# Performance work log

Measured on AMD Instinct MI355X. Metric: run time of the kernel, lower is better.

Reference implementation:

```python
import jax, jax.numpy as jnp
import numpy as np
from jax import lax

H = 12  # num_heads

def conv1d_same(x, w, b):
    # x: [B, Cin, L], w: [Cout, Cin, K] (torch Conv1d layout), 'same' padding
    y = lax.conv_general_dilated(x, w, window_strides=(1,), padding='SAME',
                                 dimension_numbers=('NCH', 'OIH', 'NCH'))
    return y + b[None, :, None]

def setup_inputs() -> dict:
    key = jax.random.key(0)
    ks = jax.random.split(key, 16)
    B, N, C = 8, 4096, 768
    d = C // H
    s = 0.02
    return {
        'x': jax.random.normal(ks[0], (B, N, C), dtype=jnp.float32),
        'qkv_w': jax.random.normal(ks[1], (3 * C, C), dtype=jnp.float32) * s,
        'proj_w': jax.random.normal(ks[2], (C, C), dtype=jnp.float32) * s,
        'proj_b': jnp.zeros((C,), dtype=jnp.float32),
        'conv_w': jax.random.normal(ks[3], (d, d, 5), dtype=jnp.float32) * s,  # k=5 from log2(768)
        'conv_b': jnp.zeros((d,), dtype=jnp.float32),
        'fc_w': jax.random.normal(ks[4], (d, d), dtype=jnp.float32) * s,
        'fc_b': jnp.zeros((d,), dtype=jnp.float32),
        'dw1_w': jax.random.normal(ks[5], (d, d, 3), dtype=jnp.float32) * s,
        'dw1_b': jnp.zeros((d,), dtype=jnp.float32),
        'dw2_w': jax.random.normal(ks[6], (d, d, 5), dtype=jnp.float32) * s,
        'dw2_b': jnp.zeros((d,), dtype=jnp.float32),
    }

def reference(x, qkv_w, proj_w, proj_b, conv_w, conv_b, fc_w, fc_b, dw1_w, dw1_b, dw2_w, dw2_b):
    B, N, C = x.shape
    d = C // H
    scale = d ** (-0.5)
    # qkv projection -> [3, B, H, N, d]
    qkv = (x @ qkv_w.T).reshape(B, N, 3, H, d).transpose(2, 0, 3, 1, 4)
    q, k, v = qkv[0], qkv[1], qkv[2]
    # SE-style gate: global avg over tokens, conv over channel axis, sigmoid
    res = jnp.mean(v, axis=2).reshape(B * H, d, 1)          # [BH, d, 1]
    res = conv1d_same(res, conv_w, conv_b)                   # [BH, d, 1]
    res = jax.nn.sigmoid(res).transpose(0, 2, 1).reshape(B, H, 1, d)
    # value branch: two 1D convs over token axis (channels = head_dim)
    vch = v.reshape(B * H, N, d).transpose(0, 2, 1)          # [BH, d, N]
    v2 = conv1d_same(vch, dw1_w, dw1_b) + conv1d_same(vch, dw2_w, dw2_b)
    v2 = v2.transpose(0, 2, 1).reshape(B, H, N, d)
    # channel attention: (scaled k)^T @ q -> [B, H, d, d]
    kq = jnp.einsum('bhnd,bhne->bhde', k * scale, q)
    a = jax.nn.relu(kq) @ fc_w.T + fc_b
    a = jax.nn.softmax(a + kq, axis=-1)
    # (a @ v2^T)^T -> [B, H, N, d]
    out = jnp.einsum('bhde,bhne->bhnd', a, v2)
    out = res * out
    out = out.transpose(0, 2, 1, 3).reshape(B, N, C)
    return out @ proj_w.T + proj_b
```

## Files before the change

### kernel.cpp

```cpp
#include <hip/hip_runtime.h>
#include <hip/hip_bf16.h>
#include <cstdint>
#include <cstddef>

typedef unsigned short u16;
typedef __attribute__((ext_vector_type(4))) unsigned short u16x4;
typedef __attribute__((ext_vector_type(8))) unsigned short u16x8;
typedef __attribute__((ext_vector_type(8))) short bf16x8;
typedef __attribute__((ext_vector_type(4))) float f32x4;

#define BB 8
#define NN 4096
#define CC 768
#define HH 12
#define DD 64
#define NHEADS 96
#define QKVSZ 25165824LL

__device__ inline float b2f(u16 u) { return __uint_as_float(((unsigned)u) << 16); }
__device__ inline u16 f2b(float f) {
    unsigned u = __float_as_uint(f);
    return (u16)((u + 0x7fffu + ((u >> 16) & 1u)) >> 16);
}
__device__ inline f32x4 zero4() { f32x4 z = {0.f, 0.f, 0.f, 0.f}; return z; }

__global__ void cast_f32_bf16(const float* __restrict__ src, u16* __restrict__ dst, int n) {
    long i0 = (long)(blockIdx.x * blockDim.x + threadIdx.x) * 4;
    long stride = (long)gridDim.x * blockDim.x * 4;
    for (long j = i0; j < n; j += stride) {
        float4 v = *(const float4*)(src + j);
        u16x4 o;
        o[0] = f2b(v.x); o[1] = f2b(v.y); o[2] = f2b(v.z); o[3] = f2b(v.w);
        *(u16x4*)(dst + j) = o;
    }
}

template <int MODE>
__global__ __launch_bounds__(256) void gemm128(const u16* __restrict__ A, const u16* __restrict__ Bm,
                                               const float* __restrict__ bias, void* __restrict__ out) {
    constexpr int K = 768;
    __shared__ __align__(16) u16 lA[128 * 64];
    __shared__ __align__(16) u16 lB[128 * 64];
    const int tid = threadIdx.x;
    const int row0 = blockIdx.x * 128;
    const int col0 = blockIdx.y * 128;
    const int lane = tid & 63, wid = tid >> 6;
    const int wr = wid >> 1, wc = wid & 1;
    const int sr = tid >> 3, sc = (tid & 7) * 8;

    f32x4 acc[4][4];
#pragma unroll
    for (int i = 0; i < 4; ++i)
#pragma unroll
        for (int j = 0; j < 4; ++j) acc[i][j] = zero4();

    for (int kt = 0; kt < K; kt += 64) {
#pragma unroll
        for (int p = 0; p < 4; ++p) {
            int r = sr + p * 32;
            *(u16x8*)((char*)lA + ((r * 128 + sc * 2) ^ ((r & 7) << 4))) =
                *(const u16x8*)(A + (size_t)(row0 + r) * K + kt + sc);
            *(u16x8*)((char*)lB + ((r * 128 + sc * 2) ^ ((r & 7) << 4))) =
                *(const u16x8*)(Bm + (size_t)(col0 + r) * K + kt + sc);
        }
        __syncthreads();
#pragma unroll
        for (int kk = 0; kk < 64; kk += 32) {
            int kc = kk * 2 + ((lane >> 4) << 4);
            bf16x8 af[4], bf_[4];
#pragma unroll
            for (int i = 0; i < 4; ++i) {
                int ra = wr * 64 + i * 16 + (lane & 15);
                af[i] = *(const bf16x8*)((char*)lA + ((ra * 128 + kc) ^ ((ra & 7) << 4)));
                int rb = wc * 64 + i * 16 + (lane & 15);
                bf_[i] = *(const bf16x8*)((char*)lB + ((rb * 128 + kc) ^ ((rb & 7) << 4)));
            }
#pragma unroll
            for (int i = 0; i < 4; ++i)
#pragma unroll
                for (int j = 0; j < 4; ++j)
                    acc[i][j] = __builtin_amdgcn_mfma_f32_16x16x32_bf16(af[i], bf_[j], acc[i][j], 0, 0, 0);
        }
        __syncthreads();
    }

    const int g = lane >> 4, li = lane & 15;
#pragma unroll
    for (int i = 0; i < 4; ++i) {
#pragma unroll
        for (int j = 0; j < 4; ++j) {
            int c = col0 + wc * 64 + j * 16 + li;
            if constexpr (MODE == 0) {
                int part = c / 768, rem = c % 768;
                int h = rem >> 6, dd = rem & 63;
#pragma unroll
                for (int e = 0; e < 4; ++e) {
                    int r = row0 + wr * 64 + i * 16 + g * 4 + e;
                    int b = r >> 12, n = r & 4095;
                    ((u16*)out)[(((size_t)part * NHEADS + b * HH + h) * NN + n) * DD + dd] =
                        f2b(acc[i][j][e]);
                }
            } else {
                float bb = bias[c];
#pragma unroll
                for (int e = 0; e < 4; ++e) {
                    int r = row0 + wr * 64 + i * 16 + g * 4 + e;
                    ((float*)out)[(size_t)r * 768 + c] = acc[i][j][e] + bb;
                }
            }
        }
    }
}

__global__ __launch_bounds__(256) void mean_partial(const u16* __restrict__ qkv, float* __restrict__ meanp) {
    const int head = blockIdx.x, c = blockIdx.y;
    const int tid = threadIdx.x;
    const u16* vh = qkv + 2 * QKVSZ + (size_t)head * NN * DD;
    __shared__ float sred[16 * 64];
    int rg = tid >> 4, cg = tid & 15;
    int n0 = c * 256;
    float s0 = 0.f, s1 = 0.f, s2 = 0.f, s3 = 0.f;
#pragma unroll 4
    for (int it = 0; it < 16; ++it) {
        int n = n0 + rg + it * 16;
        u16x4 v = *(const u16x4*)(vh + (size_t)n * DD + cg * 4);
        s0 += b2f(v[0]); s1 += b2f(v[1]); s2 += b2f(v[2]); s3 += b2f(v[3]);
    }
    sred[rg * 64 + cg * 4 + 0] = s0;
    sred[rg * 64 + cg * 4 + 1] = s1;
    sred[rg * 64 + cg * 4 + 2] = s2;
    sred[rg * 64 + cg * 4 + 3] = s3;
    __syncthreads();
    if (tid < 64) {
        float s = 0.f;
#pragma unroll
        for (int rg2 = 0; rg2 < 16; ++rg2) s += sred[rg2 * 64 + tid];
        meanp[((size_t)head * 16 + c) * 64 + tid] = s;
    }
}

__global__ __launch_bounds__(256) void kq_partial(const u16* __restrict__ qkv, float* __restrict__ kqp) {
    const int head = blockIdx.x, part = blockIdx.y;
    const int tid = threadIdx.x, lane = tid & 63, wid = tid >> 6;
    __shared__ __align__(16) u16 tiles[4][2][32 * 64];
    u16* kt = tiles[wid][0];
    u16* qt = tiles[wid][1];
    const u16* qh = qkv + (size_t)head * NN * DD;
    const u16* kh = qkv + QKVSZ + (size_t)head * NN * DD;
    const int nbase = part * 1024 + wid * 256;

    f32x4 acc[4][4];
#pragma unroll
    for (int i = 0; i < 4; ++i)
#pragma unroll
        for (int j = 0; j < 4; ++j) acc[i][j] = zero4();

    const int srow = lane >> 3, schunk = (lane & 7) * 8;
    const int g8 = (lane >> 4) * 8, li = lane & 15;

    for (int it = 0; it < 8; ++it) {
        int n0 = nbase + it * 32;
#pragma unroll
        for (int p = 0; p < 4; ++p) {
            int r = srow + p * 8;
            *(u16x8*)(kt + r * 64 + schunk) = *(const u16x8*)(kh + (size_t)(n0 + r) * DD + schunk);
            *(u16x8*)(qt + r * 64 + schunk) = *(const u16x8*)(qh + (size_t)(n0 + r) * DD + schunk);
        }
        bf16x8 af[4], bf_[4];
#pragma unroll
        for (int i = 0; i < 4; ++i)
#pragma unroll
            for (int j = 0; j < 8; ++j) af[i][j] = (short)kt[(g8 + j) * 64 + i * 16 + li];
#pragma unroll
        for (int i = 0; i < 4; ++i)
#pragma unroll
            for (int j = 0; j < 8; ++j) bf_[i][j] = (short)qt[(g8 + j) * 64 + i * 16 + li];
#pragma unroll
        for (int i = 0; i < 4; ++i)
#pragma unroll
            for (int j = 0; j < 4; ++j)
                acc[i][j] = __builtin_amdgcn_mfma_f32_16x16x32_bf16(af[i], bf_[j], acc[i][j], 0, 0, 0);
    }

    const int slot = part * 4 + wid;
    const int g = lane >> 4;
    float* dst = kqp + ((size_t)head * 16 + slot) * 4096;
#pragma unroll
    for (int i = 0; i < 4; ++i)
#pragma unroll
        for (int j = 0; j < 4; ++j)
#pragma unroll
            for (int e = 0; e < 4; ++e)
                dst[(i * 16 + g * 4 + e) * 64 + j * 16 + li] = acc[i][j][e];
}

__global__ __launch_bounds__(256) void head_finish(
    const float* __restrict__ kqp, const float* __restrict__ meanp,
    const float* __restrict__ conv_w, const float* __restrict__ conv_b,
    const float* __restrict__ fc_w, const float* __restrict__ fc_b,
    const float* __restrict__ dw1_b, const float* __restrict__ dw2_b,
    float* __restrict__ sa_g, float* __restrict__ gate_g, float* __restrict__ effb) {
    const int head = blockIdx.x;
    const int tid = threadIdx.x;
    __shared__ float skq[64 * 64];
    __shared__ float sa[64 * 64];
    __shared__ float smean[64];
    __shared__ float sgate[64];

    for (int idx = tid; idx < 4096; idx += 256) {
        float s = 0.f;
#pragma unroll
        for (int p = 0; p < 16; ++p) s += kqp[((size_t)head * 16 + p) * 4096 + idx];
        skq[idx] = s * 0.125f;
    }
    if (tid < 64) {
        float s = 0.f;
#pragma unroll
        for (int p = 0; p < 16; ++p) s += meanp[((size_t)head * 16 + p) * 64 + tid];
        smean[tid] = s * (1.f / 4096.f);
    }
    __syncthreads();
    if (tid < 64) {
        float gsum = conv_b[tid];
        for (int i = 0; i < 64; ++i) gsum += conv_w[(tid * 64 + i) * 5 + 2] * smean[i];
        float gt = 1.f / (1.f + __expf(-gsum));
        sgate[tid] = gt;
        gate_g[head * 64 + tid] = gt;
    }

    {
        int rr = tid >> 2, cg = (tid & 3) * 16;
        for (int c = cg; c < cg + 16; ++c) {
            float s = fc_b[c];
            for (int e = 0; e < 64; ++e) s += fmaxf(skq[rr * 64 + e], 0.f) * fc_w[c * 64 + e];
            sa[rr * 64 + c] = s + skq[rr * 64 + c];
        }
    }
    __syncthreads();
    if (tid < 64) {
        float m = -1e30f;
        for (int e = 0; e < 64; ++e) m = fmaxf(m, sa[tid * 64 + e]);
        float s = 0.f;
        for (int e = 0; e < 64; ++e) {
            float p = __expf(sa[tid * 64 + e] - m);
            sa[tid * 64 + e] = p;
            s += p;
        }
        float inv = 1.f / s;
        for (int e = 0; e < 64; ++e) sa[tid * 64 + e] *= inv;
    }
    __syncthreads();
    for (int idx = tid; idx < 4096; idx += 256) sa_g[(size_t)head * 4096 + idx] = sa[idx];
    if (tid < 64) {
        float s = 0.f;
        for (int e = 0; e < 64; ++e) s += sa[tid * 64 + e] * (dw1_b[e] + dw2_b[e]);
        effb[head * 64 + tid] = sgate[tid] * s;
    }
}

__global__ __launch_bounds__(256) void fold_eff(
    const float* __restrict__ sa_g, const float* __restrict__ gate_g,
    const float* __restrict__ dw1_w, const float* __restrict__ dw2_w,
    u16* __restrict__ eff) {
    const int head = blockIdx.x, ig = blockIdx.y;
    const int tid = threadIdx.x;
    __shared__ float ssa[4096];
    __shared__ float sw2[64 * 16 * 5];
    __shared__ float sw1[64 * 16 * 3];

    for (int idx = tid; idx < 4096; idx += 256) ssa[idx] = sa_g[(size_t)head * 4096 + idx];
    for (int idx = tid; idx < 64 * 16 * 5; idx += 256) {
        int e = idx / 80, rem = idx % 80, il = rem / 5, t = rem % 5;
        sw2[idx] = dw2_w[((size_t)(e * 64 + ig * 16 + il)) * 5 + t];
    }
    for (int idx = tid; idx < 64 * 16 * 3; idx += 256) {
        int e = idx / 48, rem = idx % 48, il = rem / 3, t = rem % 3;
        sw1[idx] = dw1_w[((size_t)(e * 64 + ig * 16 + il)) * 3 + t];
    }
    __syncthreads();

    const int il = tid & 15, og = tid >> 4;
    const int i = ig * 16 + il;
    float t[4][5];
#pragma unroll
    for (int o = 0; o < 4; ++o)
#pragma unroll
        for (int tp = 0; tp < 5; ++tp) t[o][tp] = 0.f;

    for (int e = 0; e < 64; ++e) {
        float a0 = ssa[(og * 4 + 0) * 64 + e];
        float a1 = ssa[(og * 4 + 1) * 64 + e];
        float a2 = ssa[(og * 4 + 2) * 64 + e];
        float a3 = ssa[(og * 4 + 3) * 64 + e];
        const float* w2 = sw2 + (e * 16 + il) * 5;
        const float* w1 = sw1 + (e * 16 + il) * 3;
        float c0 = w2[0], c1 = w2[1] + w1[0], c2 = w2[2] + w1[1], c3 = w2[3] + w1[2], c4 = w2[4];
        t[0][0] += a0 * c0; t[0][1] += a0 * c1; t[0][2] += a0 * c2; t[0][3] += a0 * c3; t[0][4] += a0 * c4;
        t[1][0] += a1 * c0; t[1][1] += a1 * c1; t[1][2] += a1 * c2; t[1][3] += a1 * c3; t[1][4] += a1 * c4;
        t[2][0] += a2 * c0; t[2][1] += a2 * c1; t[2][2] += a2 * c2; t[2][3] += a2 * c3; t[2][4] += a2 * c4;
        t[3][0] += a3 * c0; t[3][1] += a3 * c1; t[3][2] += a3 * c2; t[3][3] += a3 * c3; t[3][4] += a3 * c4;
    }
#pragma unroll
    for (int o = 0; o < 4; ++o) {
        int oo = og * 4 + o;
        float gt = gate_g[head * 64 + oo];
        u16* eo = eff + ((size_t)head * 64 + oo) * 320 + i;
#pragma unroll
        for (int tp = 0; tp < 5; ++tp) eo[tp * 64] = f2b(gt * t[o][tp]);
    }
}

__global__ __launch_bounds__(256) void conv_attn(const u16* __restrict__ qkv, const u16* __restrict__ eff,
                                                 const float* __restrict__ effb, u16* __restrict__ attn) {
    const int nt = blockIdx.x, head = blockIdx.y;
    const int tid = threadIdx.x, lane = tid & 63, wid = tid >> 6;
    __shared__ __align__(16) u16 vt[132 * 64];
    const int n0 = nt * 128;
    const u16* vh = qkv + 2 * QKVSZ + (size_t)head * NN * DD;

    {
        int sr = tid >> 3, sc = (tid & 7) * 8;
#pragma unroll
        for (int p = 0; p < 5; ++p) {
            int r = sr + p * 32;
            if (r < 132) {
                int n = n0 - 2 + r;
                u16x8 v = {0, 0, 0, 0, 0, 0, 0, 0};
                if (n >= 0 && n < NN) v = *(const u16x8*)(vh + (size_t)n * DD + sc);
                *(u16x8*)((char*)vt + ((r * 128 + sc * 2) ^ ((r & 7) << 4))) = v;
            }
        }
    }
    __syncthreads();

    f32x4 acc[2][4];
#pragma unroll
    for (int s = 0; s < 2; ++s)
#pragma unroll
        for (int j = 0; j < 4; ++j) acc[s][j] = zero4();

    const u16* effh = eff + (size_t)head * 64 * 320;
    const int li = lane & 15, g = lane >> 4;
#pragma unroll
    for (int s = 0; s < 10; ++s) {
        int tap = s >> 1, half = s & 1;
        bf16x8 bfr[4];
#pragma unroll
        for (int nj = 0; nj < 4; ++nj)
            bfr[nj] = *(const bf16x8*)(effh + (size_t)(nj * 16 + li) * 320 + s * 32 + g * 8);
        int kc = half * 64 + g * 16;
#pragma unroll
        for (int sub = 0; sub < 2; ++sub) {
            int rr = wid * 32 + sub * 16 + li + tap;
            bf16x8 afr = *(const bf16x8*)((char*)vt + ((rr * 128 + kc) ^ ((rr & 7) << 4)));
#pragma unroll
            for (int nj = 0; nj < 4; ++nj)
                acc[sub][nj] = __builtin_amdgcn_mfma_f32_16x16x32_bf16(afr, bfr[nj], acc[sub][nj], 0, 0, 0);
        }
    }

    const int b = head / HH, h = head % HH;
#pragma unroll
    for (int sub = 0; sub < 2; ++sub)
#pragma unroll
        for (int nj = 0; nj < 4; ++nj) {
            int o = nj * 16 + li;
            float bb = effb[head * 64 + o];
#pragma unroll
            for (int e = 0; e < 4; ++e) {
                int m = wid * 32 + sub * 16 + g * 4 + e;
                size_t n = (size_t)n0 + m;
                attn[((size_t)b * NN + n) * CC + h * DD + o] = f2b(acc[sub][nj][e] + bb);
            }
        }
}

extern "C" void kernel_launch(void* const* d_in, const int* in_sizes, int n_in,
                              void* d_out, int out_size, void* d_ws, size_t ws_size,
                              hipStream_t stream) {
    const float* x      = (const float*)d_in[0];
    const float* qkv_w  = (const float*)d_in[1];
    const float* proj_w = (const float*)d_in[2];
    const float* proj_b = (const float*)d_in[3];
    const float* conv_w = (const float*)d_in[4];
    const float* conv_b = (const float*)d_in[5];
    const float* fc_w   = (const float*)d_in[6];
    const float* fc_b   = (const float*)d_in[7];
    const float* dw1_w  = (const float*)d_in[8];
    const float* dw1_b  = (const float*)d_in[9];
    const float* dw2_w  = (const float*)d_in[10];
    const float* dw2_b  = (const float*)d_in[11];

    char* ws = (char*)d_ws;
    u16* xb    = (u16*)(ws);
    u16* wqkv  = (u16*)(ws + 50331648);
    u16* wproj = (u16*)(ws + 53870592);
    u16* qkv   = (u16*)(ws + 55050240);
    u16* eff   = (u16*)(ws + 206045184);
    float* effb = (float*)(ws + 209977344);
    u16* attn  = (u16*)(ws + 210001920);

    float* kqp   = (float*)(ws);
    float* meanp = (float*)(ws + 25165824);
    float* sa_g  = (float*)(ws + 25559040);
    float* gate_g = (float*)(ws + 27131904);

    float* out = (float*)d_out;

    cast_f32_bf16<<<1024, 256, 0, stream>>>(x, xb, BB * NN * CC);
    cast_f32_bf16<<<256, 256, 0, stream>>>(qkv_w, wqkv, 3 * CC * CC);
    cast_f32_bf16<<<256, 256, 0, stream>>>(proj_w, wproj, CC * CC);

    gemm128<0><<<dim3(256, 18), 256, 0, stream>>>(xb, wqkv, nullptr, qkv);

    mean_partial<<<dim3(96, 16), 256, 0, stream>>>(qkv, meanp);
    kq_partial<<<dim3(96, 4), 256, 0, stream>>>(qkv, kqp);
    head_finish<<<96, 256, 0, stream>>>(kqp, meanp, conv_w, conv_b, fc_w, fc_b,
                                        dw1_b, dw2_b, sa_g, gate_g, effb);
    fold_eff<<<dim3(96, 4), 256, 0, stream>>>(sa_g, gate_g, dw1_w, dw2_w, eff);

    conv_attn<<<dim3(32, 96), 256, 0, stream>>>(qkv, eff, effb, attn);

    gemm128<1><<<dim3(256, 6), 256, 0, stream>>>(attn, wproj, proj_b, out);
}
```

Baseline: 418.3 us.

## Use direct global-to-LDS loads with XCD swizzle in GEMMs and fuse small head kernels

```diff
diff --git a/kernel.cpp b/kernel.cpp
--- a/kernel.cpp
+++ b/kernel.cpp
@@ -23,6 +23,12 @@
     return (u16)((u + 0x7fffu + ((u >> 16) & 1u)) >> 16);
 }
 __device__ inline f32x4 zero4() { f32x4 z = {0.f, 0.f, 0.f, 0.f}; return z; }
+
+__device__ __forceinline__ void gl_lds16(const u16* g, u16* l) {
+    __builtin_amdgcn_global_load_lds(
+        (const __attribute__((address_space(1))) void*)g,
+        (__attribute__((address_space(3))) void*)l, 16, 0, 0);
+}
 
 __global__ void cast_f32_bf16(const float* __restrict__ src, u16* __restrict__ dst, int n) {
     long i0 = (long)(blockIdx.x * blockDim.x + threadIdx.x) * 4;
@@ -36,17 +42,22 @@
 }
 
 template <int MODE>
-__global__ __launch_bounds__(256) void gemm128(const u16* __restrict__ A, const u16* __restrict__ Bm,
-                                               const float* __restrict__ bias, void* __restrict__ out) {
+__global__ __launch_bounds__(256) void gemm128g(const u16* __restrict__ A, const u16* __restrict__ Bm,
+                                                const float* __restrict__ bias, void* __restrict__ out,
+                                                int nby) {
     constexpr int K = 768;
     __shared__ __align__(16) u16 lA[128 * 64];
     __shared__ __align__(16) u16 lB[128 * 64];
     const int tid = threadIdx.x;
-    const int row0 = blockIdx.x * 128;
-    const int col0 = blockIdx.y * 128;
     const int lane = tid & 63, wid = tid >> 6;
     const int wr = wid >> 1, wc = wid & 1;
-    const int sr = tid >> 3, sc = (tid & 7) * 8;
+    const int li = lane & 15, g = lane >> 4;
+
+    const int nwg = gridDim.x;
+    const int chunk = nwg >> 3;
+    const int swz = (blockIdx.x & 7) * chunk + (blockIdx.x >> 3);
+    const int row0 = (swz / nby) * 128;
+    const int col0 = (swz % nby) * 128;
 
     f32x4 acc[4][4];
 #pragma unroll
@@ -54,26 +65,24 @@
 #pragma unroll
         for (int j = 0; j < 4; ++j) acc[i][j] = zero4();
 
+    const int lrow = lane >> 3;
+    const int lcol = (lane & 7) * 8;
+
     for (int kt = 0; kt < K; kt += 64) {
 #pragma unroll
-        for (int p = 0; p < 4; ++p) {
-            int r = sr + p * 32;
-            *(u16x8*)((char*)lA + ((r * 128 + sc * 2) ^ ((r & 7) << 4))) =
-                *(const u16x8*)(A + (size_t)(row0 + r) * K + kt + sc);
-            *(u16x8*)((char*)lB + ((r * 128 + sc * 2) ^ ((r & 7) << 4))) =
-                *(const u16x8*)(Bm + (size_t)(col0 + r) * K + kt + sc);
+        for (int s = 0; s < 4; ++s) {
+            int r0 = wid * 32 + s * 8;
+            gl_lds16(A + (size_t)(row0 + r0 + lrow) * K + kt + lcol, lA + r0 * 64);
+            gl_lds16(Bm + (size_t)(col0 + r0 + lrow) * K + kt + lcol, lB + r0 * 64);
         }
         __syncthreads();
 #pragma unroll
         for (int kk = 0; kk < 64; kk += 32) {
-            int kc = kk * 2 + ((lane >> 4) << 4);
             bf16x8 af[4], bf_[4];
 #pragma unroll
             for (int i = 0; i < 4; ++i) {
-                int ra = wr * 64 + i * 16 + (lane & 15);
-                af[i] = *(const bf16x8*)((char*)lA + ((ra * 128 + kc) ^ ((ra & 7) << 4)));
-                int rb = wc * 64 + i * 16 + (lane & 15);
-                bf_[i] = *(const bf16x8*)((char*)lB + ((rb * 128 + kc) ^ ((rb & 7) << 4)));
+                af[i]  = *(const bf16x8*)(lA + (wr * 64 + i * 16 + li) * 64 + kk + g * 8);
+                bf_[i] = *(const bf16x8*)(lB + (wc * 64 + i * 16 + li) * 64 + kk + g * 8);
             }
 #pragma unroll
             for (int i = 0; i < 4; ++i)
@@ -84,7 +93,6 @@
         __syncthreads();
     }
 
-    const int g = lane >> 4, li = lane & 15;
 #pragma unroll
     for (int i = 0; i < 4; ++i) {
 #pragma unroll
@@ -112,37 +120,36 @@
     }
 }
 
-__global__ __launch_bounds__(256) void mean_partial(const u16* __restrict__ qkv, float* __restrict__ meanp) {
-    const int head = blockIdx.x, c = blockIdx.y;
-    const int tid = threadIdx.x;
-    const u16* vh = qkv + 2 * QKVSZ + (size_t)head * NN * DD;
-    __shared__ float sred[16 * 64];
-    int rg = tid >> 4, cg = tid & 15;
-    int n0 = c * 256;
-    float s0 = 0.f, s1 = 0.f, s2 = 0.f, s3 = 0.f;
-#pragma unroll 4
-    for (int it = 0; it < 16; ++it) {
-        int n = n0 + rg + it * 16;
-        u16x4 v = *(const u16x4*)(vh + (size_t)n * DD + cg * 4);
-        s0 += b2f(v[0]); s1 += b2f(v[1]); s2 += b2f(v[2]); s3 += b2f(v[3]);
-    }
-    sred[rg * 64 + cg * 4 + 0] = s0;
-    sred[rg * 64 + cg * 4 + 1] = s1;
-    sred[rg * 64 + cg * 4 + 2] = s2;
-    sred[rg * 64 + cg * 4 + 3] = s3;
-    __syncthreads();
-    if (tid < 64) {
-        float s = 0.f;
-#pragma unroll
-        for (int rg2 = 0; rg2 < 16; ++rg2) s += sred[rg2 * 64 + tid];
-        meanp[((size_t)head * 16 + c) * 64 + tid] = s;
-    }
-}
-
-__global__ __launch_bounds__(256) void kq_partial(const u16* __restrict__ qkv, float* __restrict__ kqp) {
+__global__ __launch_bounds__(256) void kq_mean(const u16* __restrict__ qkv, float* __restrict__ kqp,
+                                               float* __restrict__ meanp) {
     const int head = blockIdx.x, part = blockIdx.y;
     const int tid = threadIdx.x, lane = tid & 63, wid = tid >> 6;
     __shared__ __align__(16) u16 tiles[4][2][32 * 64];
+    __shared__ float sred[16 * 64];
+
+    if (part == 4) {
+        const u16* vh = qkv + 2 * QKVSZ + (size_t)head * NN * DD;
+        int rg = tid >> 4, cg = tid & 15;
+        float s0 = 0.f, s1 = 0.f, s2 = 0.f, s3 = 0.f;
+        for (int it = 0; it < 256; ++it) {
+            int n = rg + it * 16;
+            u16x4 v = *(const u16x4*)(vh + (size_t)n * DD + cg * 4);
+            s0 += b2f(v[0]); s1 += b2f(v[1]); s2 += b2f(v[2]); s3 += b2f(v[3]);
+        }
+        sred[rg * 64 + cg * 4 + 0] = s0;
+        sred[rg * 64 + cg * 4 + 1] = s1;
+        sred[rg * 64 + cg * 4 + 2] = s2;
+        sred[rg * 64 + cg * 4 + 3] = s3;
+        __syncthreads();
+        if (tid < 64) {
+            float s = 0.f;
+#pragma unroll
+            for (int rg2 = 0; rg2 < 16; ++rg2) s += sred[rg2 * 64 + tid];
+            meanp[head * 64 + tid] = s;
+        }
+        return;
+    }
+
     u16* kt = tiles[wid][0];
     u16* qt = tiles[wid][1];
     const u16* qh = qkv + (size_t)head * NN * DD;
@@ -198,34 +205,29 @@
     const float* __restrict__ kqp, const float* __restrict__ meanp,
     const float* __restrict__ conv_w, const float* __restrict__ conv_b,
     const float* __restrict__ fc_w, const float* __restrict__ fc_b,
-    const float* __restrict__ dw1_b, const float* __restrict__ dw2_b,
-    float* __restrict__ sa_g, float* __restrict__ gate_g, float* __restrict__ effb) {
+    const float* __restrict__ dw1_w, const float* __restrict__ dw1_b,
+    const float* __restrict__ dw2_w, const float* __restrict__ dw2_b,
+    u16* __restrict__ eff, float* __restrict__ effb) {
     const int head = blockIdx.x;
     const int tid = threadIdx.x;
     __shared__ float skq[64 * 64];
     __shared__ float sa[64 * 64];
-    __shared__ float smean[64];
     __shared__ float sgate[64];
+    __shared__ float sw2[64 * 16 * 5];
+    __shared__ float sw1[64 * 16 * 3];
 
     for (int idx = tid; idx < 4096; idx += 256) {
         float s = 0.f;
 #pragma unroll
         for (int p = 0; p < 16; ++p) s += kqp[((size_t)head * 16 + p) * 4096 + idx];
         skq[idx] = s * 0.125f;
-    }
-    if (tid < 64) {
-        float s = 0.f;
-#pragma unroll
-        for (int p = 0; p < 16; ++p) s += meanp[((size_t)head * 16 + p) * 64 + tid];
-        smean[tid] = s * (1.f / 4096.f);
     }
     __syncthreads();
     if (tid < 64) {
         float gsum = conv_b[tid];
-        for (int i = 0; i < 64; ++i) gsum += conv_w[(tid * 64 + i) * 5 + 2] * smean[i];
-        float gt = 1.f / (1.f + __expf(-gsum));
-        sgate[tid] = gt;
-        gate_g[head * 64 + tid] = gt;
+        for (int i = 0; i < 64; ++i)
+            gsum += conv_w[(tid * 64 + i) * 5 + 2] * (meanp[head * 64 + i] * (1.f / 4096.f));
+        sgate[tid] = 1.f / (1.f + __expf(-gsum));
     }
 
     {
@@ -250,63 +252,53 @@
         for (int e = 0; e < 64; ++e) sa[tid * 64 + e] *= inv;
     }
     __syncthreads();
-    for (int idx = tid; idx < 4096; idx += 256) sa_g[(size_t)head * 4096 + idx] = sa[idx];
     if (tid < 64) {
         float s = 0.f;
         for (int e = 0; e < 64; ++e) s += sa[tid * 64 + e] * (dw1_b[e] + dw2_b[e]);
         effb[head * 64 + tid] = sgate[tid] * s;
     }
-}
-
-__global__ __launch_bounds__(256) void fold_eff(
-    const float* __restrict__ sa_g, const float* __restrict__ gate_g,
-    const float* __restrict__ dw1_w, const float* __restrict__ dw2_w,
-    u16* __restrict__ eff) {
-    const int head = blockIdx.x, ig = blockIdx.y;
-    const int tid = threadIdx.x;
-    __shared__ float ssa[4096];
-    __shared__ float sw2[64 * 16 * 5];
-    __shared__ float sw1[64 * 16 * 3];
-
-    for (int idx = tid; idx < 4096; idx += 256) ssa[idx] = sa_g[(size_t)head * 4096 + idx];
-    for (int idx = tid; idx < 64 * 16 * 5; idx += 256) {
-        int e = idx / 80, rem = idx % 80, il = rem / 5, t = rem % 5;
-        sw2[idx] = dw2_w[((size_t)(e * 64 + ig * 16 + il)) * 5 + t];
-    }
-    for (int idx = tid; idx < 64 * 16 * 3; idx += 256) {
-        int e = idx / 48, rem = idx % 48, il = rem / 3, t = rem % 3;
-        sw1[idx] = dw1_w[((size_t)(e * 64 + ig * 16 + il)) * 3 + t];
-    }
-    __syncthreads();
-
-    const int il = tid & 15, og = tid >> 4;
-    const int i = ig * 16 + il;
-    float t[4][5];
-#pragma unroll
-    for (int o = 0; o < 4; ++o)
-#pragma unroll
-        for (int tp = 0; tp < 5; ++tp) t[o][tp] = 0.f;
-
-    for (int e = 0; e < 64; ++e) {
-        float a0 = ssa[(og * 4 + 0) * 64 + e];
-        float a1 = ssa[(og * 4 + 1) * 64 + e];
-        float a2 = ssa[(og * 4 + 2) * 64 + e];
-        float a3 = ssa[(og * 4 + 3) * 64 + e];
-        const float* w2 = sw2 + (e * 16 + il) * 5;
-        const float* w1 = sw1 + (e * 16 + il) * 3;
-        float c0 = w2[0], c1 = w2[1] + w1[0], c2 = w2[2] + w1[1], c3 = w2[3] + w1[2], c4 = w2[4];
-        t[0][0] += a0 * c0; t[0][1] += a0 * c1; t[0][2] += a0 * c2; t[0][3] += a0 * c3; t[0][4] += a0 * c4;
-        t[1][0] += a1 * c0; t[1][1] += a1 * c1; t[1][2] += a1 * c2; t[1][3] += a1 * c3; t[1][4] += a1 * c4;
-        t[2][0] += a2 * c0; t[2][1] += a2 * c1; t[2][2] += a2 * c2; t[2][3] += a2 * c3; t[2][4] += a2 * c4;
-        t[3][0] += a3 * c0; t[3][1] += a3 * c1; t[3][2] += a3 * c2; t[3][3] += a3 * c3; t[3][4] += a3 * c4;
-    }
-#pragma unroll
-    for (int o = 0; o < 4; ++o) {
-        int oo = og * 4 + o;
-        float gt = gate_g[head * 64 + oo];
-        u16* eo = eff + ((size_t)head * 64 + oo) * 320 + i;
-#pragma unroll
-        for (int tp = 0; tp < 5; ++tp) eo[tp * 64] = f2b(gt * t[o][tp]);
+
+    for (int ig = 0; ig < 4; ++ig) {
+        __syncthreads();
+        for (int idx = tid; idx < 64 * 16 * 5; idx += 256) {
+            int e = idx / 80, rem = idx % 80, il2 = rem / 5, t = rem % 5;
+            sw2[idx] = dw2_w[((size_t)(e * 64 + ig * 16 + il2)) * 5 + t];
+        }
+        for (int idx = tid; idx < 64 * 16 * 3; idx += 256) {
+            int e = idx / 48, rem = idx % 48, il2 = rem / 3, t = rem % 3;
+            sw1[idx] = dw1_w[((size_t)(e * 64 + ig * 16 + il2)) * 3 + t];
+        }
+        __syncthreads();
+
+        const int il = tid & 15, og = tid >> 4;
+        const int i = ig * 16 + il;
+        float t[4][5];
+#pragma unroll
+        for (int o = 0; o < 4; ++o)
+#pragma unroll
+            for (int tp = 0; tp < 5; ++tp) t[o][tp] = 0.f;
+
+        for (int e = 0; e < 64; ++e) {
+            float a0 = sa[(og * 4 + 0) * 64 + e];
+            float a1 = sa[(og * 4 + 1) * 64 + e];
+            float a2 = sa[(og * 4 + 2) * 64 + e];
+            float a3 = sa[(og * 4 + 3) * 64 + e];
+            const float* w2 = sw2 + (e * 16 + il) * 5;
+            const float* w1 = sw1 + (e * 16 + il) * 3;
+            float c0 = w2[0], c1 = w2[1] + w1[0], c2 = w2[2] + w1[1], c3 = w2[3] + w1[2], c4 = w2[4];
+            t[0][0] += a0 * c0; t[0][1] += a0 * c1; t[0][2] += a0 * c2; t[0][3] += a0 * c3; t[0][4] += a0 * c4;
+            t[1][0] += a1 * c0; t[1][1] += a1 * c1; t[1][2] += a1 * c2; t[1][3] += a1 * c3; t[1][4] += a1 * c4;
+            t[2][0] += a2 * c0; t[2][1] += a2 * c1; t[2][2] += a2 * c2; t[2][3] += a2 * c3; t[2][4] += a2 * c4;
+            t[3][0] += a3 * c0; t[3][1] += a3 * c1; t[3][2] += a3 * c2; t[3][3] += a3 * c3; t[3][4] += a3 * c4;
+        }
+#pragma unroll
+        for (int o = 0; o < 4; ++o) {
+            int oo = og * 4 + o;
+            float gt = sgate[oo];
+            u16* eo = eff + ((size_t)head * 64 + oo) * 320 + i;
+#pragma unroll
+            for (int tp = 0; tp < 5; ++tp) eo[tp * 64] = f2b(gt * t[o][tp]);
+        }
     }
 }
 
@@ -402,8 +394,6 @@
 
     float* kqp   = (float*)(ws);
     float* meanp = (float*)(ws + 25165824);
-    float* sa_g  = (float*)(ws + 25559040);
-    float* gate_g = (float*)(ws + 27131904);
 
     float* out = (float*)d_out;
 
@@ -411,15 +401,13 @@
     cast_f32_bf16<<<256, 256, 0, stream>>>(qkv_w, wqkv, 3 * CC * CC);
     cast_f32_bf16<<<256, 256, 0, stream>>>(proj_w, wproj, CC * CC);
 
-    gemm128<0><<<dim3(256, 18), 256, 0, stream>>>(xb, wqkv, nullptr, qkv);
-
-    mean_partial<<<dim3(96, 16), 256, 0, stream>>>(qkv, meanp);
-    kq_partial<<<dim3(96, 4), 256, 0, stream>>>(qkv, kqp);
+    gemm128g<0><<<4608, 256, 0, stream>>>(xb, wqkv, nullptr, qkv, 18);
+
+    kq_mean<<<dim3(96, 5), 256, 0, stream>>>(qkv, kqp, meanp);
     head_finish<<<96, 256, 0, stream>>>(kqp, meanp, conv_w, conv_b, fc_w, fc_b,
-                                        dw1_b, dw2_b, sa_g, gate_g, effb);
-    fold_eff<<<dim3(96, 4), 256, 0, stream>>>(sa_g, gate_g, dw1_w, dw2_w, eff);
+                                        dw1_w, dw1_b, dw2_w, dw2_b, eff, effb);
 
     conv_attn<<<dim3(32, 96), 256, 0, stream>>>(qkv, eff, effb, attn);
 
-    gemm128<1><<<dim3(256, 6), 256, 0, stream>>>(attn, wproj, proj_b, out);
-}
+    gemm128g<1><<<1536, 256, 0, stream>>>(attn, wproj, proj_b, out, 6);
+}
```

After: 486.6 us. 16.3% more time.
